# Kernel optimization log

Hardware: AMD Instinct MI355X
Metric: run time of the kernel (lower is better)

The kernel has to match this reference:

```python
import jax, jax.numpy as jnp
import numpy as np

K = 32  # neighbors per query point


def _gather_points(x, idx):
    # x: [B, N, D], idx: [B, M, k] -> [B, M, k, D]
    B, M, k = idx.shape
    D = x.shape[-1]
    flat = jnp.take_along_axis(x, idx.reshape(B, M * k, 1), axis=1)
    return flat.reshape(B, M, k, D)


def setup_inputs() -> dict:
    key = jax.random.key(0)
    k1, k2, k3, k4, k5 = jax.random.split(key, 5)
    B, N, M, Cin = 16, 4096, 1024, 64
    pos = jax.random.normal(k1, (B, N, 3), dtype=jnp.float32)
    features = jax.random.normal(k2, (B, N, Cin), dtype=jnp.float32)
    idx = jax.random.randint(k3, (B, M), 0, N, dtype=jnp.int64)
    # 1x1 conv2d MLP params: (Cin+3) -> 64 -> 128 (use_xyz adds 3 channels)
    W1 = jax.random.normal(k4, (Cin + 3, 64), dtype=jnp.float32) * (1.0 / np.sqrt(Cin + 3))
    b1 = jnp.zeros((64,), dtype=jnp.float32)
    W2 = jax.random.normal(k5, (64, 128), dtype=jnp.float32) * (1.0 / np.sqrt(64))
    b2 = jnp.zeros((128,), dtype=jnp.float32)
    return {"pos": pos, "features": features, "W1": W1, "b1": b1,
            "W2": W2, "b2": b2, "idx": idx}


def reference(pos, features, W1, b1, W2, b2, idx):
    # pos: [B,N,3], features: [B,N,C], idx: [B,M] query-point indices
    pos_q = jnp.take_along_axis(pos, idx[..., None], axis=1)  # [B,M,3]
    # squared-distance knn: [B,M,N]
    d2 = (jnp.sum(pos_q ** 2, -1, keepdims=True)
          + jnp.sum(pos ** 2, -1)[:, None, :]
          - 2.0 * jnp.einsum("bmd,bnd->bmn", pos_q, pos))
    _, nn_idx = jax.lax.top_k(-d2, K)  # [B,M,K] nearest neighbors
    grouped_pos = _gather_points(pos, nn_idx)          # [B,M,K,3]
    grouped_feat = _gather_points(features, nn_idx)    # [B,M,K,C]
    rel = grouped_pos - pos_q[:, :, None, :]           # recenter groups
    x = jnp.concatenate([rel, grouped_feat], axis=-1)  # [B,M,K,C+3] (use_xyz)
    # 1x1 conv2d MLP == per-point linear + ReLU on channel dim
    h = jax.nn.relu(jnp.einsum("bmkc,cd->bmkd", x, W1) + b1)
    h = jax.nn.relu(jnp.einsum("bmkc,cd->bmkd", h, W2) + b2)
    out = jnp.max(h, axis=-2)  # max over K neighbors -> [B,M,128]
    return (pos_q, out)
```

## Files before the change

kernel.cpp:

```cpp
#include <hip/hip_runtime.h>

#define NPTS  4096
#define MQ    1024
#define BATCH 16
#define KNN   32
#define CIN   64
#define H1D   64
#define H2D   128

typedef _Float16 half8 __attribute__((ext_vector_type(8)));
typedef float    floatx4 __attribute__((ext_vector_type(4)));

#define W1F_HALVES  (3 * 4 * 64 * 8)
#define W2F_HALVES  (2 * 8 * 64 * 8)
#define WS_WF_BYTES ((size_t)(W1F_HALVES + W2F_HALVES) * 2)
#define WS_P4_OFF   WS_WF_BYTES
#define WS_F16_OFF  (WS_P4_OFF + (size_t)BATCH * NPTS * 16)
#define WS_NEED     (WS_F16_OFF + (size_t)BATCH * NPTS * CIN * 2)

__global__ __launch_bounds__(256) void wprep_kernel(
    const float* __restrict__ W1, const float* __restrict__ W2,
    const float* __restrict__ pos, const float* __restrict__ feat,
    _Float16* __restrict__ wout, float4* __restrict__ pos4,
    _Float16* __restrict__ feat16, int do_f16)
{
    const int gid = blockIdx.x * 256 + threadIdx.x;
    if (gid < 768) {
        const int s = gid;
        const int kc = s >> 8, nt = (s >> 6) & 3, lane = s & 63;
        const int col = lane & 15, quad = lane >> 4;
        half8 ph;
#pragma unroll
        for (int j = 0; j < 8; ++j) {
            const int k = kc * 32 + quad * 8 + j;
            ph[j] = (k < 67) ? (_Float16)W1[k * H1D + nt * 16 + col] : (_Float16)0.0f;
        }
        *(half8*)(wout + (size_t)s * 8) = ph;
    } else if (gid < 1792) {
        const int s2 = gid - 768;
        const int kc2 = s2 >> 9, nt2 = (s2 >> 6) & 7, lane = s2 & 63;
        const int col = lane & 15, quad = lane >> 4;
        half8 ph;
#pragma unroll
        for (int j = 0; j < 8; ++j) {
            const int k = kc2 * 32 + quad * 8 + j;
            ph[j] = (_Float16)W2[k * H2D + nt2 * 16 + col];
        }
        *(half8*)(wout + (size_t)W1F_HALVES + (size_t)s2 * 8) = ph;
    } else if (gid < 1792 + BATCH * NPTS) {
        const int p = gid - 1792;
        const float px = pos[p * 3 + 0], py = pos[p * 3 + 1], pz = pos[p * 3 + 2];
        float4 v;
        v.x = px; v.y = py; v.z = pz;
        v.w = __fadd_rn(__fadd_rn(__fmul_rn(px, px), __fmul_rn(py, py)),
                        __fmul_rn(pz, pz));
        pos4[p] = v;
    } else if (do_f16) {
        const int s = gid - (1792 + BATCH * NPTS);
        if (s < BATCH * NPTS * 8) {
            const int row = s >> 3, c8 = (s & 7) * 8;
            const float4* fp = (const float4*)(feat + (size_t)row * CIN + c8);
            const float4 a = fp[0], c = fp[1];
            half8 h;
            h[0] = (_Float16)a.x; h[1] = (_Float16)a.y;
            h[2] = (_Float16)a.z; h[3] = (_Float16)a.w;
            h[4] = (_Float16)c.x; h[5] = (_Float16)c.y;
            h[6] = (_Float16)c.z; h[7] = (_Float16)c.w;
            *(half8*)(feat16 + (size_t)row * CIN + c8) = h;
        }
    }
}

template<int USE_F16>
__global__ __launch_bounds__(256, 4) void fused_kernel(
    const float4* __restrict__ pos4, const float* __restrict__ feat,
    const _Float16* __restrict__ feat16, const int* __restrict__ idx,
    const float* __restrict__ b1, const float* __restrict__ b2,
    const _Float16* __restrict__ wf,
    float* __restrict__ pos_q, float* __restrict__ out)
{
    __shared__ unsigned int histS[4 * 2048];
    __shared__ unsigned int ckeyS[4][64];
    __shared__ int          cidxS[4][64];
    __shared__ int          nnLDS[4][KNN];
    __shared__ unsigned int scS[4][8];
    __shared__ unsigned int wsumS[4][4];
    _Float16* sh = (_Float16*)histS;

    const int t = threadIdx.x;
    const int w = t >> 6, lane = t & 63;
    const int qblk = blockIdx.x * 4;
    const int b = qblk >> 10;
    const float4* pb4 = pos4 + (size_t)b * NPTS;

    float4 qvv[4];
#pragma unroll
    for (int qi = 0; qi < 4; ++qi)
        qvv[qi] = pb4[idx[(size_t)b * MQ + ((qblk & (MQ - 1)) + qi)]];

    {
        int4* hz = (int4*)histS;
        const int4 z = make_int4(0, 0, 0, 0);
#pragma unroll
        for (int j = 0; j < 8; ++j) hz[t + 256 * j] = z;
    }
    __syncthreads();

    unsigned int k[4][16];
    {
        float4 pr[4];
#pragma unroll
        for (int i = 0; i < 4; ++i) pr[i] = pb4[i * 256 + t];
#pragma unroll
        for (int i = 0; i < 16; ++i) {
            const float4 p = pr[i & 3];
            if (i < 12) pr[i & 3] = pb4[(i + 4) * 256 + t];
#pragma unroll
            for (int qi = 0; qi < 4; ++qi) {
                const float qp = __fadd_rn(__fadd_rn(__fmul_rn(qvv[qi].x, p.x),
                                                     __fmul_rn(qvv[qi].y, p.y)),
                                           __fmul_rn(qvv[qi].z, p.z));
                const float d2 = __fsub_rn(__fadd_rn(qvv[qi].w, p.w),
                                           __fmul_rn(2.0f, qp));
                unsigned int u = __float_as_uint(d2);
                u = (u & 0x80000000u) ? ~u : (u | 0x80000000u);
                k[qi][i] = u;
                atomicAdd(&histS[(qi << 11) | (u >> 21)], 1u);
            }
        }
    }
    __syncthreads();

    unsigned int sq[4], vq[4];
#pragma unroll
    for (int qi = 0; qi < 4; ++qi) {
        unsigned int s = 0;
#pragma unroll
        for (int j = 0; j < 8; ++j) s += histS[(qi << 11) + t * 8 + j];
        unsigned int v = s;
#pragma unroll
        for (int off = 1; off < 64; off <<= 1) {
            const unsigned int o = __shfl_up(v, off);
            if (lane >= off) v += o;
        }
        if (lane == 63) wsumS[qi][w] = v;
        sq[qi] = s; vq[qi] = v;
    }
    __syncthreads();
#pragma unroll
    for (int qi = 0; qi < 4; ++qi) {
        unsigned int woff = 0;
#pragma unroll
        for (int i = 0; i < 4; ++i) if (i < w) woff += wsumS[qi][i];
        const unsigned int incl = woff + vq[qi], excl = incl - sq[qi];
        const unsigned int rank0 = KNN - 1;
        if (rank0 >= excl && rank0 < incl) {
            unsigned int e = excl;
            for (int j = 0; j < 8; ++j) {
                const unsigned int c = histS[(qi << 11) + t * 8 + j];
                if (rank0 < e + c) {
                    scS[qi][0] = (unsigned int)(t * 8 + j);
                    scS[qi][1] = rank0 - e;
                    scS[qi][2] = c;
                    break;
                }
                e += c;
            }
        }
    }
    __syncthreads();

    unsigned int prefq[4], rankq[4]; int shiftq[4];
#pragma unroll
    for (int qi = 0; qi < 4; ++qi) {
        prefq[qi] = scS[qi][0];
        rankq[qi] = scS[qi][1];
        shiftq[qi] = 21;
    }

#pragma unroll
    for (int qi = 0; qi < 4; ++qi) {
        if (scS[qi][2] > 64) {
            for (int lvl = 1; lvl < 3; ++lvl) {
                const int nb  = (lvl == 1) ? 11 : 10;
                const int sh2 = (lvl == 1) ? 10 : 0;
                const unsigned int msk = (1u << nb) - 1u;
                const int g = (1 << nb) >> 8;
                for (int j = 0; j < g; ++j) histS[(qi << 11) + t * g + j] = 0u;
                __syncthreads();
#pragma unroll
                for (int i = 0; i < 16; ++i) {
                    const unsigned int u = k[qi][i];
                    if ((u >> (sh2 + nb)) == prefq[qi])
                        atomicAdd(&histS[(qi << 11) + ((u >> sh2) & msk)], 1u);
                }
                __syncthreads();
                unsigned int cnt[8];
                unsigned int s = 0;
                for (int j = 0; j < g; ++j) { cnt[j] = histS[(qi << 11) + t * g + j]; s += cnt[j]; }
                unsigned int v = s;
#pragma unroll
                for (int off = 1; off < 64; off <<= 1) {
                    const unsigned int o = __shfl_up(v, off);
                    if (lane >= off) v += o;
                }
                if (lane == 63) wsumS[qi][w] = v;
                __syncthreads();
                unsigned int woff = 0;
#pragma unroll
                for (int i2 = 0; i2 < 4; ++i2) if (i2 < w) woff += wsumS[qi][i2];
                const unsigned int incl = woff + v, excl = incl - s;
                const unsigned int r = rankq[qi];
                if (r >= excl && r < incl) {
                    unsigned int e = excl;
                    for (int j = 0; j < g; ++j) {
                        if (r < e + cnt[j]) {
                            scS[qi][0] = (prefq[qi] << nb) | (unsigned int)(t * g + j);
                            scS[qi][1] = r - e;
                            scS[qi][2] = cnt[j];
                            break;
                        }
                        e += cnt[j];
                    }
                }
                __syncthreads();
                prefq[qi] = scS[qi][0];
                rankq[qi] = scS[qi][1];
                shiftq[qi] = sh2;
                if (scS[qi][2] <= 64u || lvl == 2) break;
            }
        }
    }

    if (t < 4) { scS[t][3] = 0u; scS[t][4] = 0u; }
    __syncthreads();
#pragma unroll
    for (int i = 0; i < 16; ++i) {
        const int n = i * 256 + t;
#pragma unroll
        for (int qi = 0; qi < 4; ++qi) {
            const unsigned int u = k[qi][i];
            const unsigned int hp = u >> shiftq[qi];
            if (hp < prefq[qi]) {
                const unsigned int slot = atomicAdd(&scS[qi][3], 1u);
                if (slot < KNN) nnLDS[qi][slot] = n;
            } else if (hp == prefq[qi]) {
                const unsigned int slot = atomicAdd(&scS[qi][4], 1u);
                if (slot < 64u) { ckeyS[qi][slot] = u; cidxS[qi][slot] = n; }
            }
        }
    }
    __syncthreads();

    {
        const int candcnt = min((int)scS[w][4], 64);
        const int defcnt  = min((int)scS[w][3], KNN);
        const int rnk     = (int)scS[w][1];
        const unsigned int k_l = (lane < candcnt) ? ckeyS[w][lane] : 0xFFFFFFFFu;
        const int          i_l = (lane < candcnt) ? cidxS[w][lane] : 0x7FFFFFFF;
        int rk = 0;
        for (int j = 0; j < candcnt; ++j) {
            const unsigned int kj = __shfl(k_l, j);
            const int          ij = __shfl(i_l, j);
            if (kj < k_l || (kj == k_l && ij < i_l)) ++rk;
        }
        if (lane < candcnt && rk <= rnk && defcnt + rk < KNN)
            nnLDS[w][defcnt + rk] = i_l;
    }
    if (t < 4) {
        const float4 qv = (t == 0) ? qvv[0] : (t == 1) ? qvv[1] : (t == 2) ? qvv[2] : qvv[3];
        pos_q[(size_t)(qblk + t) * 3 + 0] = qv.x;
        pos_q[(size_t)(qblk + t) * 3 + 1] = qv.y;
        pos_q[(size_t)(qblk + t) * 3 + 2] = qv.z;
    }
    __syncthreads();

    const int q = qblk + w;
    const int wbase = w * 3072;
    const float4 qme = (w == 0) ? qvv[0] : (w == 1) ? qvv[1] : (w == 2) ? qvv[2] : qvv[3];

    {
        const int r = t >> 1, h = t & 1;
        const int kk = r & 31;
        const int n = nnLDS[w][kk];
        const int mt = kk >> 4, lrow = kk & 15;
        if (USE_F16) {
            const _Float16* frow = feat16 + ((size_t)b * NPTS + n) * CIN;
            if (h == 0) {
                const float4 pv = pos4[(size_t)b * NPTS + n];
                half8 fa[6];
#pragma unroll
                for (int ii = 0; ii < 6; ++ii) fa[ii] = *(const half8*)(frow + ii * 8);
                float relf[3] = {pv.x - qme.x, pv.y - qme.y, pv.z - qme.z};
#pragma unroll
                for (int ci = 0; ci < 6; ++ci) {
                    half8 ph;
#pragma unroll
                    for (int jj = 0; jj < 8; ++jj) {
                        const int c = ci * 8 + jj;
                        ph[jj] = (c < 3) ? (_Float16)relf[c] : fa[(c - 3) >> 3][(c - 3) & 7];
                    }
                    const int kc = ci >> 2, qd = ci & 3;
                    *(half8*)&sh[wbase + ((kc * 2 + mt) * 64 + qd * 16 + lrow) * 8] = ph;
                }
            } else {
                half8 fb[3];
#pragma unroll
                for (int ii = 0; ii < 3; ++ii) fb[ii] = *(const half8*)(frow + 40 + ii * 8);
#pragma unroll
                for (int ci = 6; ci < 12; ++ci) {
                    half8 ph;
#pragma unroll
                    for (int jj = 0; jj < 8; ++jj) {
                        const int c = ci * 8 + jj;
                        _Float16 v = (_Float16)0.0f;
                        if (c < 67) { const int f = c - 43; v = fb[f >> 3][f & 7]; }
                        ph[jj] = v;
                    }
                    const int kc = ci >> 2, qd = ci & 3;
                    *(half8*)&sh[wbase + ((kc * 2 + mt) * 64 + qd * 16 + lrow) * 8] = ph;
                }
            }
        } else {
            const float4* f4 = (const float4*)(feat + ((size_t)b * NPTS + n) * CIN);
            if (h == 0) {
                const float4 pv = pos4[(size_t)b * NPTS + n];
                float4 ff[12];
#pragma unroll
                for (int ii = 0; ii < 12; ++ii) ff[ii] = f4[ii];
                float relf[3] = {pv.x - qme.x, pv.y - qme.y, pv.z - qme.z};
#pragma unroll
                for (int ci = 0; ci < 6; ++ci) {
                    half8 ph;
#pragma unroll
                    for (int jj = 0; jj < 8; ++jj) {
                        const int c = ci * 8 + jj;
                        float v;
                        if (c < 3) v = relf[c];
                        else {
                            const int fc = c - 3;
                            const float4 vv = ff[fc >> 2];
                            v = ((fc & 3) == 0) ? vv.x : ((fc & 3) == 1) ? vv.y
                              : ((fc & 3) == 2) ? vv.z : vv.w;
                        }
                        ph[jj] = (_Float16)v;
                    }
                    const int kc = ci >> 2, qd = ci & 3;
                    *(half8*)&sh[wbase + ((kc * 2 + mt) * 64 + qd * 16 + lrow) * 8] = ph;
                }
            } else {
                float4 ff[5];
#pragma unroll
                for (int ii = 0; ii < 5; ++ii) ff[ii] = f4[11 + ii];
#pragma unroll
                for (int ci = 6; ci < 12; ++ci) {
                    half8 ph;
#pragma unroll
                    for (int jj = 0; jj < 8; ++jj) {
                        const int c = ci * 8 + jj;
                        float v = 0.0f;
                        if (c < 67) {
                            const int fc = c - 3;
                            const float4 vv = ff[(fc >> 2) - 11];
                            v = ((fc & 3) == 0) ? vv.x : ((fc & 3) == 1) ? vv.y
                              : ((fc & 3) == 2) ? vv.z : vv.w;
                        }
                        ph[jj] = (_Float16)v;
                    }
                    const int kc = ci >> 2, qd = ci & 3;
                    *(half8*)&sh[wbase + ((kc * 2 + mt) * 64 + qd * 16 + lrow) * 8] = ph;
                }
            }
        }
    }

    const int col = lane & 15, quad = lane >> 4;

    half8 af[3][2];
#pragma unroll
    for (int kc = 0; kc < 3; ++kc)
#pragma unroll
        for (int mt = 0; mt < 2; ++mt)
            af[kc][mt] = *(const half8*)&sh[wbase + ((kc * 2 + mt) * 64 + lane) * 8];

    half8 w1f[3][4];
#pragma unroll
    for (int kc = 0; kc < 3; ++kc)
#pragma unroll
        for (int nt = 0; nt < 4; ++nt)
            w1f[kc][nt] = *(const half8*)(wf + (size_t)((kc * 4 + nt) * 64 + lane) * 8);

#pragma unroll
    for (int nt = 0; nt < 4; ++nt) {
        const float bv = b1[nt * 16 + col];
        floatx4 acc0 = {bv, bv, bv, bv}, acc1 = acc0;
#pragma unroll
        for (int kc = 0; kc < 3; ++kc) {
            acc0 = __builtin_amdgcn_mfma_f32_16x16x32_f16(af[kc][0], w1f[kc][nt], acc0, 0, 0, 0);
            acc1 = __builtin_amdgcn_mfma_f32_16x16x32_f16(af[kc][1], w1f[kc][nt], acc1, 0, 0, 0);
        }
        const int kc2 = nt >> 1;
        const int quad2 = (((nt & 1) * 16) + col) >> 3;
        const int j2 = col & 7;
#pragma unroll
        for (int mt = 0; mt < 2; ++mt) {
            const floatx4 a = mt ? acc1 : acc0;
#pragma unroll
            for (int reg = 0; reg < 4; ++reg) {
                const int row = quad * 4 + reg;
                sh[wbase + ((kc2 * 2 + mt) * 64 + quad2 * 16 + row) * 8 + j2] =
                    (_Float16)fmaxf(a[reg], 0.0f);
            }
        }
    }

    half8 a2[2][2];
#pragma unroll
    for (int kc2 = 0; kc2 < 2; ++kc2)
#pragma unroll
        for (int mt = 0; mt < 2; ++mt)
            a2[kc2][mt] = *(const half8*)&sh[wbase + ((kc2 * 2 + mt) * 64 + lane) * 8];

    half8 w2f[2][8];
#pragma unroll
    for (int kc2 = 0; kc2 < 2; ++kc2)
#pragma unroll
        for (int nt2 = 0; nt2 < 8; ++nt2)
            w2f[kc2][nt2] = *(const half8*)(wf + (size_t)W1F_HALVES
                                            + (size_t)((kc2 * 8 + nt2) * 64 + lane) * 8);

    float* oq = out + (size_t)q * H2D;
#pragma unroll
    for (int nt2 = 0; nt2 < 8; ++nt2) {
        const float bv = b2[nt2 * 16 + col];
        floatx4 acc0 = {bv, bv, bv, bv}, acc1 = acc0;
#pragma unroll
        for (int kc2 = 0; kc2 < 2; ++kc2) {
            acc0 = __builtin_amdgcn_mfma_f32_16x16x32_f16(a2[kc2][0], w2f[kc2][nt2], acc0, 0, 0, 0);
            acc1 = __builtin_amdgcn_mfma_f32_16x16x32_f16(a2[kc2][1], w2f[kc2][nt2], acc1, 0, 0, 0);
        }
        float mm = fmaxf(fmaxf(fmaxf(acc0[0], acc0[1]), fmaxf(acc0[2], acc0[3])),
                         fmaxf(fmaxf(acc1[0], acc1[1]), fmaxf(acc1[2], acc1[3])));
        mm = fmaxf(mm, 0.0f);
        mm = fmaxf(mm, __shfl_xor(mm, 16));
        mm = fmaxf(mm, __shfl_xor(mm, 32));
        if (lane < 16) oq[nt2 * 16 + lane] = mm;
    }
}

extern "C" void kernel_launch(void* const* d_in, const int* in_sizes, int n_in,
                              void* d_out, int out_size, void* d_ws, size_t ws_size,
                              hipStream_t stream)
{
    const float* pos  = (const float*)d_in[0];
    const float* feat = (const float*)d_in[1];
    const float* W1   = (const float*)d_in[2];
    const float* b1   = (const float*)d_in[3];
    const float* W2   = (const float*)d_in[4];
    const float* b2   = (const float*)d_in[5];
    const int*   idx  = (const int*)d_in[6];

    float* pos_q = (float*)d_out;
    float* out   = (float*)d_out + (size_t)BATCH * MQ * 3;
    _Float16* wf  = (_Float16*)d_ws;
    float4*   p4  = (float4*)((char*)d_ws + WS_P4_OFF);
    _Float16* f16 = (_Float16*)((char*)d_ws + WS_F16_OFF);

    const int use_f16 = (ws_size >= WS_NEED) ? 1 : 0;
    const int prep_threads = 1792 + BATCH * NPTS + (use_f16 ? BATCH * NPTS * 8 : 0);
    wprep_kernel<<<(prep_threads + 255) / 256, 256, 0, stream>>>(
        W1, W2, pos, feat, wf, p4, f16, use_f16);
    if (use_f16)
        fused_kernel<1><<<BATCH * MQ / 4, 256, 0, stream>>>(
            p4, feat, f16, idx, b1, b2, wf, pos_q, out);
    else
        fused_kernel<0><<<BATCH * MQ / 4, 256, 0, stream>>>(
            p4, feat, f16, idx, b1, b2, wf, pos_q, out);
}
```

Before: 200.5 us.

## Recompute distance keys instead of caching, drop fp16 feature preconversion

```diff
diff --git a/kernel.cpp b/kernel.cpp
--- a/kernel.cpp
+++ b/kernel.cpp
@@ -15,14 +15,20 @@
 #define W2F_HALVES  (2 * 8 * 64 * 8)
 #define WS_WF_BYTES ((size_t)(W1F_HALVES + W2F_HALVES) * 2)
 #define WS_P4_OFF   WS_WF_BYTES
-#define WS_F16_OFF  (WS_P4_OFF + (size_t)BATCH * NPTS * 16)
-#define WS_NEED     (WS_F16_OFF + (size_t)BATCH * NPTS * CIN * 2)
+
+__device__ __forceinline__ unsigned int d2key(const float4 q, const float4 p)
+{
+    const float qp = __fadd_rn(__fadd_rn(__fmul_rn(q.x, p.x), __fmul_rn(q.y, p.y)),
+                               __fmul_rn(q.z, p.z));
+    const float d2 = __fsub_rn(__fadd_rn(q.w, p.w), __fmul_rn(2.0f, qp));
+    unsigned int u = __float_as_uint(d2);
+    return (u & 0x80000000u) ? ~u : (u | 0x80000000u);
+}
 
 __global__ __launch_bounds__(256) void wprep_kernel(
     const float* __restrict__ W1, const float* __restrict__ W2,
-    const float* __restrict__ pos, const float* __restrict__ feat,
-    _Float16* __restrict__ wout, float4* __restrict__ pos4,
-    _Float16* __restrict__ feat16, int do_f16)
+    const float* __restrict__ pos,
+    _Float16* __restrict__ wout, float4* __restrict__ pos4)
 {
     const int gid = blockIdx.x * 256 + threadIdx.x;
     if (gid < 768) {
@@ -55,26 +61,12 @@
         v.w = __fadd_rn(__fadd_rn(__fmul_rn(px, px), __fmul_rn(py, py)),
                         __fmul_rn(pz, pz));
         pos4[p] = v;
-    } else if (do_f16) {
-        const int s = gid - (1792 + BATCH * NPTS);
-        if (s < BATCH * NPTS * 8) {
-            const int row = s >> 3, c8 = (s & 7) * 8;
-            const float4* fp = (const float4*)(feat + (size_t)row * CIN + c8);
-            const float4 a = fp[0], c = fp[1];
-            half8 h;
-            h[0] = (_Float16)a.x; h[1] = (_Float16)a.y;
-            h[2] = (_Float16)a.z; h[3] = (_Float16)a.w;
-            h[4] = (_Float16)c.x; h[5] = (_Float16)c.y;
-            h[6] = (_Float16)c.z; h[7] = (_Float16)c.w;
-            *(half8*)(feat16 + (size_t)row * CIN + c8) = h;
-        }
     }
 }
 
-template<int USE_F16>
 __global__ __launch_bounds__(256, 4) void fused_kernel(
     const float4* __restrict__ pos4, const float* __restrict__ feat,
-    const _Float16* __restrict__ feat16, const int* __restrict__ idx,
+    const int* __restrict__ idx,
     const float* __restrict__ b1, const float* __restrict__ b2,
     const _Float16* __restrict__ wf,
     float* __restrict__ pos_q, float* __restrict__ out)
@@ -106,7 +98,6 @@
     }
     __syncthreads();
 
-    unsigned int k[4][16];
     {
         float4 pr[4];
 #pragma unroll
@@ -117,14 +108,7 @@
             if (i < 12) pr[i & 3] = pb4[(i + 4) * 256 + t];
 #pragma unroll
             for (int qi = 0; qi < 4; ++qi) {
-                const float qp = __fadd_rn(__fadd_rn(__fmul_rn(qvv[qi].x, p.x),
-                                                     __fmul_rn(qvv[qi].y, p.y)),
-                                           __fmul_rn(qvv[qi].z, p.z));
-                const float d2 = __fsub_rn(__fadd_rn(qvv[qi].w, p.w),
-                                           __fmul_rn(2.0f, qp));
-                unsigned int u = __float_as_uint(d2);
-                u = (u & 0x80000000u) ? ~u : (u | 0x80000000u);
-                k[qi][i] = u;
+                const unsigned int u = d2key(qvv[qi], p);
                 atomicAdd(&histS[(qi << 11) | (u >> 21)], 1u);
             }
         }
@@ -188,9 +172,9 @@
                 const int g = (1 << nb) >> 8;
                 for (int j = 0; j < g; ++j) histS[(qi << 11) + t * g + j] = 0u;
                 __syncthreads();
-#pragma unroll
                 for (int i = 0; i < 16; ++i) {
-                    const unsigned int u = k[qi][i];
+                    const float4 p = pb4[i * 256 + t];
+                    const unsigned int u = d2key(qvv[qi], p);
                     if ((u >> (sh2 + nb)) == prefq[qi])
                         atomicAdd(&histS[(qi << 11) + ((u >> sh2) & msk)], 1u);
                 }
@@ -237,9 +221,10 @@
 #pragma unroll
     for (int i = 0; i < 16; ++i) {
         const int n = i * 256 + t;
+        const float4 p = pb4[n];
 #pragma unroll
         for (int qi = 0; qi < 4; ++qi) {
-            const unsigned int u = k[qi][i];
+            const unsigned int u = d2key(qvv[qi], p);
             const unsigned int hp = u >> shiftq[qi];
             if (hp < prefq[qi]) {
                 const unsigned int slot = atomicAdd(&scS[qi][3], 1u);
@@ -284,92 +269,53 @@
         const int kk = r & 31;
         const int n = nnLDS[w][kk];
         const int mt = kk >> 4, lrow = kk & 15;
-        if (USE_F16) {
-            const _Float16* frow = feat16 + ((size_t)b * NPTS + n) * CIN;
-            if (h == 0) {
-                const float4 pv = pos4[(size_t)b * NPTS + n];
-                half8 fa[6];
-#pragma unroll
-                for (int ii = 0; ii < 6; ++ii) fa[ii] = *(const half8*)(frow + ii * 8);
-                float relf[3] = {pv.x - qme.x, pv.y - qme.y, pv.z - qme.z};
-#pragma unroll
-                for (int ci = 0; ci < 6; ++ci) {
-                    half8 ph;
-#pragma unroll
-                    for (int jj = 0; jj < 8; ++jj) {
-                        const int c = ci * 8 + jj;
-                        ph[jj] = (c < 3) ? (_Float16)relf[c] : fa[(c - 3) >> 3][(c - 3) & 7];
+        const float4* f4 = (const float4*)(feat + ((size_t)b * NPTS + n) * CIN);
+        if (h == 0) {
+            const float4 pv = pos4[(size_t)b * NPTS + n];
+            float4 ff[12];
+#pragma unroll
+            for (int ii = 0; ii < 12; ++ii) ff[ii] = f4[ii];
+            float relf[3] = {pv.x - qme.x, pv.y - qme.y, pv.z - qme.z};
+#pragma unroll
+            for (int ci = 0; ci < 6; ++ci) {
+                half8 ph;
+#pragma unroll
+                for (int jj = 0; jj < 8; ++jj) {
+                    const int c = ci * 8 + jj;
+                    float v;
+                    if (c < 3) v = relf[c];
+                    else {
+                        const int fc = c - 3;
+                        const float4 vv = ff[fc >> 2];
+                        v = ((fc & 3) == 0) ? vv.x : ((fc & 3) == 1) ? vv.y
+                          : ((fc & 3) == 2) ? vv.z : vv.w;
                     }
-                    const int kc = ci >> 2, qd = ci & 3;
-                    *(half8*)&sh[wbase + ((kc * 2 + mt) * 64 + qd * 16 + lrow) * 8] = ph;
-                }
-            } else {
-                half8 fb[3];
-#pragma unroll
-                for (int ii = 0; ii < 3; ++ii) fb[ii] = *(const half8*)(frow + 40 + ii * 8);
-#pragma unroll
-                for (int ci = 6; ci < 12; ++ci) {
-                    half8 ph;
-#pragma unroll
-                    for (int jj = 0; jj < 8; ++jj) {
-                        const int c = ci * 8 + jj;
-                        _Float16 v = (_Float16)0.0f;
-                        if (c < 67) { const int f = c - 43; v = fb[f >> 3][f & 7]; }
-                        ph[jj] = v;
+                    ph[jj] = (_Float16)v;
+                }
+                const int kc = ci >> 2, qd = ci & 3;
+                *(half8*)&sh[wbase + ((kc * 2 + mt) * 64 + qd * 16 + lrow) * 8] = ph;
+            }
+        } else {
+            float4 ff[5];
+#pragma unroll
+            for (int ii = 0; ii < 5; ++ii) ff[ii] = f4[11 + ii];
+#pragma unroll
+            for (int ci = 6; ci < 12; ++ci) {
+                half8 ph;
+#pragma unroll
+                for (int jj = 0; jj < 8; ++jj) {
+                    const int c = ci * 8 + jj;
+                    float v = 0.0f;
+                    if (c < 67) {
+                        const int fc = c - 3;
+                        const float4 vv = ff[(fc >> 2) - 11];
+                        v = ((fc & 3) == 0) ? vv.x : ((fc & 3) == 1) ? vv.y
+                          : ((fc & 3) == 2) ? vv.z : vv.w;
                     }
-                    const int kc = ci >> 2, qd = ci & 3;
-                    *(half8*)&sh[wbase + ((kc * 2 + mt) * 64 + qd * 16 + lrow) * 8] = ph;
-                }
-            }
-        } else {
-            const float4* f4 = (const float4*)(feat + ((size_t)b * NPTS + n) * CIN);
-            if (h == 0) {
-                const float4 pv = pos4[(size_t)b * NPTS + n];
-                float4 ff[12];
-#pragma unroll
-                for (int ii = 0; ii < 12; ++ii) ff[ii] = f4[ii];
-                float relf[3] = {pv.x - qme.x, pv.y - qme.y, pv.z - qme.z};
-#pragma unroll
-                for (int ci = 0; ci < 6; ++ci) {
-                    half8 ph;
-#pragma unroll
-                    for (int jj = 0; jj < 8; ++jj) {
-                        const int c = ci * 8 + jj;
-                        float v;
-                        if (c < 3) v = relf[c];
-                        else {
-                            const int fc = c - 3;
-                            const float4 vv = ff[fc >> 2];
-                            v = ((fc & 3) == 0) ? vv.x : ((fc & 3) == 1) ? vv.y
-                              : ((fc & 3) == 2) ? vv.z : vv.w;
-                        }
-                        ph[jj] = (_Float16)v;
-                    }
-                    const int kc = ci >> 2, qd = ci & 3;
-                    *(half8*)&sh[wbase + ((kc * 2 + mt) * 64 + qd * 16 + lrow) * 8] = ph;
-                }
-            } else {
-                float4 ff[5];
-#pragma unroll
-                for (int ii = 0; ii < 5; ++ii) ff[ii] = f4[11 + ii];
-#pragma unroll
-                for (int ci = 6; ci < 12; ++ci) {
-                    half8 ph;
-#pragma unroll
-                    for (int jj = 0; jj < 8; ++jj) {
-                        const int c = ci * 8 + jj;
-                        float v = 0.0f;
-                        if (c < 67) {
-                            const int fc = c - 3;
-                            const float4 vv = ff[(fc >> 2) - 11];
-                            v = ((fc & 3) == 0) ? vv.x : ((fc & 3) == 1) ? vv.y
-                              : ((fc & 3) == 2) ? vv.z : vv.w;
-                        }
-                        ph[jj] = (_Float16)v;
-                    }
-                    const int kc = ci >> 2, qd = ci & 3;
-                    *(half8*)&sh[wbase + ((kc * 2 + mt) * 64 + qd * 16 + lrow) * 8] = ph;
-                }
+                    ph[jj] = (_Float16)v;
+                }
+                const int kc = ci >> 2, qd = ci & 3;
+                *(half8*)&sh[wbase + ((kc * 2 + mt) * 64 + qd * 16 + lrow) * 8] = ph;
             }
         }
     }
@@ -462,18 +408,11 @@
 
     float* pos_q = (float*)d_out;
     float* out   = (float*)d_out + (size_t)BATCH * MQ * 3;
-    _Float16* wf  = (_Float16*)d_ws;
-    float4*   p4  = (float4*)((char*)d_ws + WS_P4_OFF);
-    _Float16* f16 = (_Float16*)((char*)d_ws + WS_F16_OFF);
-
-    const int use_f16 = (ws_size >= WS_NEED) ? 1 : 0;
-    const int prep_threads = 1792 + BATCH * NPTS + (use_f16 ? BATCH * NPTS * 8 : 0);
-    wprep_kernel<<<(prep_threads + 255) / 256, 256, 0, stream>>>(
-        W1, W2, pos, feat, wf, p4, f16, use_f16);
-    if (use_f16)
-        fused_kernel<1><<<BATCH * MQ / 4, 256, 0, stream>>>(
-            p4, feat, f16, idx, b1, b2, wf, pos_q, out);
-    else
-        fused_kernel<0><<<BATCH * MQ / 4, 256, 0, stream>>>(
-            p4, feat, f16, idx, b1, b2, wf, pos_q, out);
+    _Float16* wf = (_Float16*)d_ws;
+    float4*   p4 = (float4*)((char*)d_ws + WS_P4_OFF);
+
+    const int prep_threads = 1792 + BATCH * NPTS;
+    wprep_kernel<<<(prep_threads + 255) / 256, 256, 0, stream>>>(W1, W2, pos, wf, p4);
+    fused_kernel<<<BATCH * MQ / 4, 256, 0, stream>>>(p4, feat, idx, b1, b2, wf,
+                                                     pos_q, out);
 }
```

After: 247.5 us. +23.4%, slower.
